# Optimization experiments

Hardware: AMD Instinct MI355X
Metric: run time of the kernel (lower is better)

The kernel has to match this reference:

```python
import jax, jax.numpy as jnp
import numpy as np

EPS = 1e-7  # K.epsilon()

def squash(v, axis=-1):
    # scale = |v|^2 / (1+|v|^2) / |v|
    ss = jnp.sum(jnp.square(v), axis=axis, keepdims=True)
    scale = ss / (1.0 + ss) / jnp.sqrt(ss + EPS)
    return scale * v

def setup_inputs() -> dict:
    key = jax.random.key(0)
    k1, k2 = jax.random.split(key)
    B, IN_CAPS, IN_DIM = 64, 512, 128
    N_CAPS, OUT_DIM = 16, 32
    inputs = jax.random.normal(k1, (B, IN_CAPS, IN_DIM), dtype=jnp.float32)
    # glorot-uniform-like init for W: (in_caps, n_caps, in_dim, out_dim)
    limit = np.sqrt(6.0 / (IN_DIM + OUT_DIM))
    W = jax.random.uniform(k2, (IN_CAPS, N_CAPS, IN_DIM, OUT_DIM),
                           minval=-limit, maxval=limit, dtype=jnp.float32)
    return {"inputs": inputs, "W": W, "num_routing": 3}

def reference(inputs, W, num_routing):
    # Prediction vectors u_hat[b,i,j,d] = sum_k inputs[b,i,k] * W[i,j,k,d]
    u_hat = jnp.einsum('bik,ijkd->bijd', inputs, W)
    B, IN_CAPS, N_CAPS, _ = u_hat.shape
    b = jnp.zeros((B, IN_CAPS, N_CAPS), dtype=u_hat.dtype)
    outputs = None
    for r in range(num_routing):  # small fixed iteration count
        c = jax.nn.softmax(b, axis=2)                     # coupling coeffs over output caps
        s = jnp.einsum('bij,bijd->bjd', c, u_hat)         # weighted sum over input caps
        outputs = squash(s)                               # (B, n_caps, out_dim)
        if r < num_routing - 1:
            b = b + jnp.einsum('bjd,bijd->bij', outputs, u_hat)  # agreement update
    return outputs
```

## Files before the change

kernel.cpp:

```cpp
#include <hip/hip_runtime.h>

typedef unsigned short u16;
typedef unsigned int u32;
typedef unsigned long long u64;
typedef __attribute__((ext_vector_type(8))) short short8;
typedef __attribute__((ext_vector_type(4))) float f32x4;

#define ICAPS 512
#define IDIM 128
#define NFLAT 512

__device__ __forceinline__ float b2f(u16 h) {
    union { u32 u; float f; } x; x.u = ((u32)h) << 16; return x.f;
}
__device__ __forceinline__ u16 f2b(float f) {
    union { float f; u32 u; } x; x.f = f;
    return (u16)((x.u + 0x7FFFu + ((x.u >> 16) & 1u)) >> 16);
}

__global__ __launch_bounds__(256, 4) void gemm_kernel(const float* __restrict__ x,
                                                      const float* __restrict__ W,
                                                      u16* __restrict__ uhat) {
    __shared__ __align__(16) u16 As[64 * 136];
    const int i = blockIdx.x >> 2;
    const int chunk = blockIdx.x & 3;
    const int t = threadIdx.x;

    {
        const float4* xa = (const float4*)x;
        float4 av[8];
        #pragma unroll
        for (int l = 0; l < 8; ++l) {
            int id = l * 256 + t;
            av[l] = xa[(size_t)((id >> 5) * ICAPS + i) * 32 + (id & 31)];
        }
        #pragma unroll
        for (int l = 0; l < 8; ++l) {
            int id = l * 256 + t;
            int row = id >> 5, kq = id & 31;
            union { u16 h[4]; u64 q; } pk;
            pk.h[0] = f2b(av[l].x); pk.h[1] = f2b(av[l].y);
            pk.h[2] = f2b(av[l].z); pk.h[3] = f2b(av[l].w);
            *(u64*)&As[row * 136 + kq * 4] = pk.q;
        }
    }
    __syncthreads();

    const int lane = t & 63;
    const int w = t >> 6;
    const int ln = lane & 15;
    const int q = lane >> 4;

    const float* colbase[2];
    #pragma unroll
    for (int nt = 0; nt < 2; ++nt) {
        int c = (2 * w + nt) * 16 + ln;
        int jj = c >> 5, d = c & 31;
        colbase[nt] = W + (size_t)(i * 16 + chunk * 4 + jj) * 128 * 32 + d;
    }

    f32x4 acc[4][2] = {};
    #pragma unroll
    for (int ks = 0; ks < 4; ++ks) {
        const int ko = ks * 32 + q * 8;
        short8 a[4], bb[2];
        #pragma unroll
        for (int mt = 0; mt < 4; ++mt)
            a[mt] = *(const short8*)&As[(mt * 16 + ln) * 136 + ko];
        #pragma unroll
        for (int nt = 0; nt < 2; ++nt) {
            const float* p = colbase[nt] + (size_t)ko * 32;
            float wv[8];
            #pragma unroll
            for (int e = 0; e < 8; ++e) wv[e] = p[e * 32];
            #pragma unroll
            for (int e = 0; e < 8; ++e) bb[nt][e] = (short)f2b(wv[e]);
        }
        #pragma unroll
        for (int mt = 0; mt < 4; ++mt)
            #pragma unroll
            for (int nt = 0; nt < 2; ++nt)
                acc[mt][nt] = __builtin_amdgcn_mfma_f32_16x16x32_bf16(a[mt], bb[nt], acc[mt][nt], 0, 0, 0);
    }
    #pragma unroll
    for (int mt = 0; mt < 4; ++mt)
        #pragma unroll
        for (int nt = 0; nt < 2; ++nt) {
            int n = chunk * 128 + (2 * w + nt) * 16 + ln;
            #pragma unroll
            for (int r = 0; r < 4; ++r) {
                int brow = mt * 16 + q * 4 + r;
                uhat[((size_t)brow * ICAPS + i) * NFLAT + n] = f2b(acc[mt][nt][r]);
            }
        }
}

__global__ __launch_bounds__(256) void p0_kernel(const u16* __restrict__ uhat,
                                                 float* __restrict__ q0) {
    __shared__ __align__(16) float red[4][NFLAT];
    const int b = blockIdx.x >> 4;
    const int ch = blockIdx.x & 15;
    const int t = threadIdx.x;
    const int wv = t >> 6, l = t & 63;
    float acc[8] = {0.f, 0.f, 0.f, 0.f, 0.f, 0.f, 0.f, 0.f};
    for (int ii = 0; ii < 8; ++ii) {
        int i = ch * 32 + wv * 8 + ii;
        union { uint4 v; u16 h[8]; } tmp;
        tmp.v = *(const uint4*)&uhat[((size_t)b * ICAPS + i) * NFLAT + l * 8];
        #pragma unroll
        for (int e = 0; e < 8; ++e) acc[e] += b2f(tmp.h[e]);
    }
    #pragma unroll
    for (int e = 0; e < 8; ++e) red[wv][l * 8 + e] = acc[e];
    __syncthreads();
    q0[(size_t)blockIdx.x * NFLAT + t] =
        red[0][t] + red[1][t] + red[2][t] + red[3][t];
    q0[(size_t)blockIdx.x * NFLAT + 256 + t] =
        red[0][t + 256] + red[1][t + 256] + red[2][t + 256] + red[3][t + 256];
}

__global__ __launch_bounds__(256) void combine_kernel(const float* __restrict__ q,
                                                      float* __restrict__ s) {
    const int b = blockIdx.x, t = threadIdx.x;
    #pragma unroll
    for (int rep = 0; rep < 2; ++rep) {
        int n = rep * 256 + t;
        float acc = 0.f;
        #pragma unroll
        for (int ch = 0; ch < 16; ++ch)
            acc += q[(size_t)(b * 16 + ch) * NFLAT + n];
        s[b * NFLAT + n] = acc;
    }
}

__device__ __forceinline__ void squash_osum(const float* __restrict__ s0,
                                            const float* __restrict__ s1,
                                            float* __restrict__ osum,
                                            int b, int t, int use1) {
    const int j = t >> 4, g = t & 15;
    const int n0 = j * 32 + 2 * g;
    float v0 = s0[b * NFLAT + n0] * 0.0625f;
    float v1 = s0[b * NFLAT + n0 + 1] * 0.0625f;
    float p = v0 * v0 + v1 * v1;
    p += __shfl_xor(p, 1); p += __shfl_xor(p, 2);
    p += __shfl_xor(p, 4); p += __shfl_xor(p, 8);
    float sc = (p / (1.f + p)) / sqrtf(p + 1e-7f);
    float o0 = sc * v0, o1 = sc * v1;
    if (use1) {
        float w0 = s1[b * NFLAT + n0];
        float w1 = s1[b * NFLAT + n0 + 1];
        float pq = w0 * w0 + w1 * w1;
        pq += __shfl_xor(pq, 1); pq += __shfl_xor(pq, 2);
        pq += __shfl_xor(pq, 4); pq += __shfl_xor(pq, 8);
        float sc1 = (pq / (1.f + pq)) / sqrtf(pq + 1e-7f);
        o0 += sc1 * w0; o1 += sc1 * w1;
    }
    osum[n0] = o0; osum[n0 + 1] = o1;
}

__global__ __launch_bounds__(256) void route_kernel(const u16* __restrict__ uhat,
                                                    const float* __restrict__ s0,
                                                    const float* __restrict__ s1,
                                                    float* __restrict__ qout,
                                                    int use1) {
    __shared__ float osum[NFLAT];
    __shared__ __align__(16) float red[4][NFLAT];
    const int b = blockIdx.x >> 4;
    const int ch = blockIdx.x & 15;
    const int t = threadIdx.x;
    squash_osum(s0, s1, osum, b, t, use1);
    __syncthreads();
    const int wv = t >> 6, l = t & 63;
    float os[8], acc[8];
    #pragma unroll
    for (int e = 0; e < 8; ++e) { os[e] = osum[l * 8 + e]; acc[e] = 0.f; }
    for (int ii = 0; ii < 8; ++ii) {
        int i = ch * 32 + wv * 8 + ii;
        union { uint4 v; u16 h[8]; } tmp;
        tmp.v = *(const uint4*)&uhat[((size_t)b * ICAPS + i) * NFLAT + l * 8];
        float u[8];
        #pragma unroll
        for (int e = 0; e < 8; ++e) u[e] = b2f(tmp.h[e]);
        float d = 0.f;
        #pragma unroll
        for (int e = 0; e < 8; ++e) d += u[e] * os[e];
        d += __shfl_xor(d, 1); d += __shfl_xor(d, 2);
        float ex = __expf(d);
        float ss = ex;
        ss += __shfl_xor(ss, 4);  ss += __shfl_xor(ss, 8);
        ss += __shfl_xor(ss, 16); ss += __shfl_xor(ss, 32);
        float c = __fdividef(ex, ss);
        #pragma unroll
        for (int e = 0; e < 8; ++e) acc[e] += c * u[e];
    }
    #pragma unroll
    for (int e = 0; e < 8; ++e) red[wv][l * 8 + e] = acc[e];
    __syncthreads();
    qout[(size_t)blockIdx.x * NFLAT + t] =
        red[0][t] + red[1][t] + red[2][t] + red[3][t];
    qout[(size_t)blockIdx.x * NFLAT + 256 + t] =
        red[0][t + 256] + red[1][t + 256] + red[2][t + 256] + red[3][t + 256];
}

__global__ __launch_bounds__(256) void fin_kernel(const float* __restrict__ q2,
                                                  float* __restrict__ out) {
    const int b = blockIdx.x, t = threadIdx.x;
    const int j = t >> 4, g = t & 15;
    const int n0 = j * 32 + 2 * g;
    float v0 = 0.f, v1 = 0.f;
    #pragma unroll
    for (int ch = 0; ch < 16; ++ch) {
        v0 += q2[(size_t)(b * 16 + ch) * NFLAT + n0];
        v1 += q2[(size_t)(b * 16 + ch) * NFLAT + n0 + 1];
    }
    float p = v0 * v0 + v1 * v1;
    p += __shfl_xor(p, 1); p += __shfl_xor(p, 2);
    p += __shfl_xor(p, 4); p += __shfl_xor(p, 8);
    float sc = (p / (1.f + p)) / sqrtf(p + 1e-7f);
    out[b * NFLAT + n0]     = sc * v0;
    out[b * NFLAT + n0 + 1] = sc * v1;
}

extern "C" void kernel_launch(void* const* d_in, const int* in_sizes, int n_in,
                              void* d_out, int out_size, void* d_ws, size_t ws_size,
                              hipStream_t stream) {
    const float* x = nullptr;
    const float* W = nullptr;
    for (int a = 0; a < n_in; ++a) {
        if (in_sizes[a] == 64 * 512 * 128) x = (const float*)d_in[a];
        else if (in_sizes[a] == 512 * 16 * 128 * 32) W = (const float*)d_in[a];
    }
    if (!x) x = (const float*)d_in[0];
    if (!W) W = (const float*)d_in[1];

    char* ws = (char*)d_ws;
    const size_t U = 2ull * 64 * 512 * 512;
    u16*   uhat = (u16*)ws;
    float* q0 = (float*)(ws + U);
    float* q1 = (float*)(ws + U + (2ull << 20));
    float* q2 = (float*)(ws + U + (4ull << 20));
    float* s0 = (float*)(ws + U + (6ull << 20));
    float* s1 = (float*)(ws + U + (6ull << 20) + (128ull << 10));
    float* out = (float*)d_out;

    hipLaunchKernelGGL(gemm_kernel, dim3(2048), dim3(256), 0, stream, x, W, uhat);
    hipLaunchKernelGGL(p0_kernel, dim3(1024), dim3(256), 0, stream, uhat, q0);
    hipLaunchKernelGGL(combine_kernel, dim3(64), dim3(256), 0, stream, q0, s0);
    hipLaunchKernelGGL(route_kernel, dim3(1024), dim3(256), 0, stream, uhat, s0, s0, q1, 0);
    hipLaunchKernelGGL(combine_kernel, dim3(64), dim3(256), 0, stream, q1, s1);
    hipLaunchKernelGGL(route_kernel, dim3(1024), dim3(256), 0, stream, uhat, s0, s1, q2, 1);
    hipLaunchKernelGGL(fin_kernel, dim3(64), dim3(256), 0, stream, q2, out);
}
```

Baseline: 240.5 us.

## Fuse partial-sum combine into route kernel and remap GEMM block order

Removes the two separate combine_kernel launches: each route block now sums the 16 per-chunk partials itself, squashes them, and caches the first-iteration squash output in a small workspace buffer for the second pass. This trades two small launches and their serialization gaps for redundant partial-sum reads, since all 16 blocks per batch re-sum the same data. The GEMM grid index is also remapped so consecutive blocks cover 8 different input capsules within one chunk, changing the order in which W and x are read, likely to improve cache locality.

After: 242.3 us. No clear change (+0.7%).

```diff
diff --git a/kernel.cpp b/kernel.cpp
--- a/kernel.cpp
+++ b/kernel.cpp
@@ -22,8 +22,9 @@
                                                       const float* __restrict__ W,
                                                       u16* __restrict__ uhat) {
     __shared__ __align__(16) u16 As[64 * 136];
-    const int i = blockIdx.x >> 2;
-    const int chunk = blockIdx.x & 3;
+    const int orig = blockIdx.x;
+    const int chunk = (orig >> 3) & 3;
+    const int i = ((orig >> 5) << 3) | (orig & 7);
     const int t = threadIdx.x;
 
     {
@@ -119,56 +120,43 @@
         red[0][t + 256] + red[1][t + 256] + red[2][t + 256] + red[3][t + 256];
 }
 
-__global__ __launch_bounds__(256) void combine_kernel(const float* __restrict__ q,
-                                                      float* __restrict__ s) {
-    const int b = blockIdx.x, t = threadIdx.x;
-    #pragma unroll
-    for (int rep = 0; rep < 2; ++rep) {
-        int n = rep * 256 + t;
-        float acc = 0.f;
-        #pragma unroll
-        for (int ch = 0; ch < 16; ++ch)
-            acc += q[(size_t)(b * 16 + ch) * NFLAT + n];
-        s[b * NFLAT + n] = acc;
-    }
-}
-
-__device__ __forceinline__ void squash_osum(const float* __restrict__ s0,
-                                            const float* __restrict__ s1,
-                                            float* __restrict__ osum,
-                                            int b, int t, int use1) {
-    const int j = t >> 4, g = t & 15;
-    const int n0 = j * 32 + 2 * g;
-    float v0 = s0[b * NFLAT + n0] * 0.0625f;
-    float v1 = s0[b * NFLAT + n0 + 1] * 0.0625f;
-    float p = v0 * v0 + v1 * v1;
-    p += __shfl_xor(p, 1); p += __shfl_xor(p, 2);
-    p += __shfl_xor(p, 4); p += __shfl_xor(p, 8);
-    float sc = (p / (1.f + p)) / sqrtf(p + 1e-7f);
-    float o0 = sc * v0, o1 = sc * v1;
-    if (use1) {
-        float w0 = s1[b * NFLAT + n0];
-        float w1 = s1[b * NFLAT + n0 + 1];
-        float pq = w0 * w0 + w1 * w1;
-        pq += __shfl_xor(pq, 1); pq += __shfl_xor(pq, 2);
-        pq += __shfl_xor(pq, 4); pq += __shfl_xor(pq, 8);
-        float sc1 = (pq / (1.f + pq)) / sqrtf(pq + 1e-7f);
-        o0 += sc1 * w0; o1 += sc1 * w1;
-    }
-    osum[n0] = o0; osum[n0 + 1] = o1;
-}
-
 __global__ __launch_bounds__(256) void route_kernel(const u16* __restrict__ uhat,
-                                                    const float* __restrict__ s0,
-                                                    const float* __restrict__ s1,
+                                                    const float* __restrict__ qin,
+                                                    float* __restrict__ osum0,
                                                     float* __restrict__ qout,
-                                                    int use1) {
+                                                    int phase) {
     __shared__ float osum[NFLAT];
     __shared__ __align__(16) float red[4][NFLAT];
     const int b = blockIdx.x >> 4;
     const int ch = blockIdx.x & 15;
     const int t = threadIdx.x;
-    squash_osum(s0, s1, osum, b, t, use1);
+    {
+        const int j = t >> 4, g = t & 15;
+        const int n0 = j * 32 + 2 * g;
+        const float* qb = qin + (size_t)(b * 16) * NFLAT;
+        float v0 = 0.f, v1 = 0.f;
+        #pragma unroll
+        for (int c2 = 0; c2 < 16; ++c2) {
+            v0 += qb[c2 * NFLAT + n0];
+            v1 += qb[c2 * NFLAT + n0 + 1];
+        }
+        if (phase == 0) { v0 *= 0.0625f; v1 *= 0.0625f; }
+        float p = v0 * v0 + v1 * v1;
+        p += __shfl_xor(p, 1); p += __shfl_xor(p, 2);
+        p += __shfl_xor(p, 4); p += __shfl_xor(p, 8);
+        float sc = (p / (1.f + p)) / sqrtf(p + 1e-7f);
+        float o0 = sc * v0, o1 = sc * v1;
+        if (phase == 0) {
+            osum[n0] = o0; osum[n0 + 1] = o1;
+            if (ch == 0) {
+                osum0[b * NFLAT + n0]     = o0;
+                osum0[b * NFLAT + n0 + 1] = o1;
+            }
+        } else {
+            osum[n0]     = o0 + osum0[b * NFLAT + n0];
+            osum[n0 + 1] = o1 + osum0[b * NFLAT + n0 + 1];
+        }
+    }
     __syncthreads();
     const int wv = t >> 6, l = t & 63;
     float os[8], acc[8];
@@ -239,15 +227,12 @@
     float* q0 = (float*)(ws + U);
     float* q1 = (float*)(ws + U + (2ull << 20));
     float* q2 = (float*)(ws + U + (4ull << 20));
-    float* s0 = (float*)(ws + U + (6ull << 20));
-    float* s1 = (float*)(ws + U + (6ull << 20) + (128ull << 10));
+    float* osum0 = (float*)(ws + U + (6ull << 20));
     float* out = (float*)d_out;
 
     hipLaunchKernelGGL(gemm_kernel, dim3(2048), dim3(256), 0, stream, x, W, uhat);
     hipLaunchKernelGGL(p0_kernel, dim3(1024), dim3(256), 0, stream, uhat, q0);
-    hipLaunchKernelGGL(combine_kernel, dim3(64), dim3(256), 0, stream, q0, s0);
-    hipLaunchKernelGGL(route_kernel, dim3(1024), dim3(256), 0, stream, uhat, s0, s0, q1, 0);
-    hipLaunchKernelGGL(combine_kernel, dim3(64), dim3(256), 0, stream, q1, s1);
-    hipLaunchKernelGGL(route_kernel, dim3(1024), dim3(256), 0, stream, uhat, s0, s1, q2, 1);
+    hipLaunchKernelGGL(route_kernel, dim3(1024), dim3(256), 0, stream, uhat, q0, osum0, q1, 0);
+    hipLaunchKernelGGL(route_kernel, dim3(1024), dim3(256), 0, stream, uhat, q1, osum0, q2, 1);
     hipLaunchKernelGGL(fin_kernel, dim3(64), dim3(256), 0, stream, q2, out);
 }
```
